# Optimization experiments

Hardware: AMD Instinct MI355X
Metric: run time of the kernel (lower is better)

Reference implementation:

```python
import jax, jax.numpy as jnp
import numpy as np

CIR_LENGTH = 64
SYM_BLK = 64
NUM_BLK = 64
H = 2 * CIR_LENGTH * SYM_BLK  # 8192, hidden size = col_num * group_size
W_SCALE = 0.01  # keep tanh out of saturation


def setup_inputs() -> dict:
    key = jax.random.key(0)
    k_x, k_ih, k_hh, k_b = jax.random.split(key, 4)
    x = jax.random.normal(k_x, (NUM_BLK, H), dtype=jnp.float32)
    W_ih = jax.random.normal(k_ih, (H, H), dtype=jnp.float32) * W_SCALE
    W_hh = jax.random.normal(k_hh, (H, H), dtype=jnp.float32) * W_SCALE
    b = jax.random.normal(k_b, (H,), dtype=jnp.float32) * W_SCALE
    return {"x": x, "W_ih": W_ih, "W_hh": W_hh, "b": b}


def reference(x, W_ih, W_hh, b):
    # Shared-weight Elman RNN over NUM_BLK blocks (the torch ModuleList holds
    # NUM copies of the SAME template module, so weights are tied).
    h0 = jnp.zeros((H,), dtype=x.dtype)

    def step(h, x_t):
        h_new = jnp.tanh(x_t @ W_ih.T + h @ W_hh.T + b)
        return h_new, h_new

    _, hs = jax.lax.scan(step, h0, x)  # hs: (NUM_BLK, H)
    # est_channel: each step's hidden reshaped to (SYM_BLK, 2*CIR_LENGTH) rows
    return hs.reshape(NUM_BLK * SYM_BLK, 2 * CIR_LENGTH)
```

## Files before the change

### kernel.cpp

```cpp
#include <hip/hip_runtime.h>
#include <cmath>
#include <type_traits>


#define HDIM 8192
#define NSTEP 64

typedef _Float16 f16;
typedef _Float16 f16x2 __attribute__((ext_vector_type(2)));
typedef _Float16 f16x4 __attribute__((ext_vector_type(4)));
typedef _Float16 f16x8 __attribute__((ext_vector_type(8)));
typedef __fp16 fp16x2_raw __attribute__((ext_vector_type(2)));
typedef float f32x4 __attribute__((ext_vector_type(4)));

#if defined(__has_builtin)
#if __has_builtin(__builtin_amdgcn_fdot2)
#define HAS_FDOT2 1
#endif
#endif

__device__ __forceinline__ f16x2 pkrtz(float a, float b) {
  fp16x2_raw r = __builtin_amdgcn_cvt_pkrtz(a, b);
  return __builtin_bit_cast(f16x2, r);
}

__device__ __forceinline__ float dot2acc(f16 a0, f16 a1, f16 b0, f16 b1, float c) {
#ifdef HAS_FDOT2
  f16x2 a = {a0, a1}, b = {b0, b1};
  return __builtin_amdgcn_fdot2(a, b, c, false);
#else
  return c + (float)a0 * (float)b0 + (float)a1 * (float)b1;
#endif
}

__global__ void cvt_f16_kernel(const float* __restrict__ src,
                               f16* __restrict__ dst, int n4) {
  int idx = blockIdx.x * blockDim.x + threadIdx.x;
  int stride = gridDim.x * blockDim.x;
  for (int i = idx; i < n4; i += stride) {
    f32x4 v = ((const f32x4*)src)[i];
    f16x4 h;
    h[0] = (f16)v[0]; h[1] = (f16)v[1]; h[2] = (f16)v[2]; h[3] = (f16)v[3];
    ((f16x4*)dst)[i] = h;
  }
}

template <bool XF16>
__global__ __launch_bounds__(256) void gemm_u_kernel(
    const float* __restrict__ x, const f16* __restrict__ x16,
    const float* __restrict__ Wih, const float* __restrict__ b,
    float* __restrict__ out) {
  const int wave = threadIdx.x >> 6;
  const int lane = threadIdx.x & 63;
  const int r = lane & 15, q = lane >> 4;
  const int n0 = blockIdx.x * 16;
  const int m0 = wave * 16;
  const float* wrow = Wih + (size_t)(n0 + r) * HDIM;
  f32x4 acc = {0.f, 0.f, 0.f, 0.f};
#pragma unroll 2
  for (int k0 = 0; k0 < HDIM; k0 += 32) {
    const int kb = k0 + q * 8;
    f16x8 fa;
    if constexpr (XF16) {
      fa = *(const f16x8*)(x16 + (size_t)(m0 + r) * HDIM + kb);
    } else {
      f32x4 a0 = *(const f32x4*)(x + (size_t)(m0 + r) * HDIM + kb);
      f32x4 a1 = *(const f32x4*)(x + (size_t)(m0 + r) * HDIM + kb + 4);
      f16x2 p0 = pkrtz(a0[0], a0[1]);
      f16x2 p1 = pkrtz(a0[2], a0[3]);
      f16x2 p2 = pkrtz(a1[0], a1[1]);
      f16x2 p3 = pkrtz(a1[2], a1[3]);
      fa = (f16x8){p0[0], p0[1], p1[0], p1[1], p2[0], p2[1], p3[0], p3[1]};
    }
    f32x4 b0 = *(const f32x4*)(wrow + kb);
    f32x4 b1 = *(const f32x4*)(wrow + kb + 4);
    f16x2 q0 = pkrtz(b0[0], b0[1]);
    f16x2 q1 = pkrtz(b0[2], b0[3]);
    f16x2 q2 = pkrtz(b1[0], b1[1]);
    f16x2 q3 = pkrtz(b1[2], b1[3]);
    f16x8 fb = {q0[0], q0[1], q1[0], q1[1], q2[0], q2[1], q3[0], q3[1]};
    acc = __builtin_amdgcn_mfma_f32_16x16x32_f16(fa, fb, acc, 0, 0, 0);
  }
  const float bv = b[n0 + r];
#pragma unroll
  for (int i = 0; i < 4; i++) {
    out[(size_t)(m0 + q * 4 + i) * HDIM + n0 + r] = acc[i] + bv;
  }
}

__global__ void step0_kernel(float* __restrict__ out) {
  int i = blockIdx.x * blockDim.x + threadIdx.x;
  out[i] = tanhf(out[i]);
}

template <bool WF16>
__global__ __launch_bounds__(1024) void step_kernel(const void* __restrict__ Wv,
                                                    float* __restrict__ out,
                                                    int t) {
  __shared__ typename std::conditional<WF16, f16, float>::type hs[HDIM];
  const float* hprev = out + (size_t)(t - 1) * HDIM;
  {
    const f32x4* hp4 = (const f32x4*)hprev;
    const int tid = threadIdx.x;
#pragma unroll
    for (int i = 0; i < HDIM / 4 / 1024; i++) {
      const int idx = i * 1024 + tid;
      f32x4 v = hp4[idx];
      if constexpr (WF16) {
        f16x4 hh;
        hh[0] = (f16)v[0]; hh[1] = (f16)v[1];
        hh[2] = (f16)v[2]; hh[3] = (f16)v[3];
        *(f16x4*)&hs[idx * 4] = hh;
      } else {
        *(f32x4*)&hs[idx * 4] = v;
      }
    }
  }
  __syncthreads();

  const int wave = threadIdx.x >> 6;
  const int lane = threadIdx.x & 63;
  const int j = blockIdx.x * 16 + wave;
  float acc = 0.f;

  if constexpr (WF16) {
    const f16* wrow = (const f16*)Wv + (size_t)j * HDIM;
#pragma unroll 4
    for (int it = 0; it < 16; it++) {
      const int kb = it * 512 + lane * 8;
      f16x8 w = *(const f16x8*)(wrow + kb);
      f16x8 h = *(const f16x8*)&hs[kb];
      acc = dot2acc(w[0], w[1], h[0], h[1], acc);
      acc = dot2acc(w[2], w[3], h[2], h[3], acc);
      acc = dot2acc(w[4], w[5], h[4], h[5], acc);
      acc = dot2acc(w[6], w[7], h[6], h[7], acc);
    }
  } else {
    const float* wrow = (const float*)Wv + (size_t)j * HDIM;
#pragma unroll 4
    for (int it = 0; it < 16; it++) {
      const int kb = it * 512 + lane * 8;
      f32x4 w0 = *(const f32x4*)(wrow + kb);
      f32x4 w1 = *(const f32x4*)(wrow + kb + 4);
      const float* hp = (const float*)&hs[kb];
      acc += w0[0] * hp[0] + w0[1] * hp[1] + w0[2] * hp[2] + w0[3] * hp[3];
      acc += w1[0] * hp[4] + w1[1] * hp[5] + w1[2] * hp[6] + w1[7 - 7 + 7] * hp[7];
    }
  }
#pragma unroll
  for (int off = 32; off >= 1; off >>= 1) acc += __shfl_down(acc, off, 64);
  if (lane == 0) {
    const float u = out[(size_t)t * HDIM + j];
    out[(size_t)t * HDIM + j] = tanhf(u + acc);
  }
}

extern "C" void kernel_launch(void* const* d_in, const int* in_sizes, int n_in,
                              void* d_out, int out_size, void* d_ws,
                              size_t ws_size, hipStream_t stream) {
  const float* x = (const float*)d_in[0];
  const float* Wih = (const float*)d_in[1];
  const float* Whh = (const float*)d_in[2];
  const float* b = (const float*)d_in[3];
  float* out = (float*)d_out;

  const size_t needW = (size_t)HDIM * HDIM * sizeof(f16);
  const size_t needX = (size_t)NSTEP * HDIM * sizeof(f16);
  const bool fast = ws_size >= needW + needX;

  if (fast) {
    f16* w16 = (f16*)d_ws;
    f16* x16 = (f16*)((char*)d_ws + needW);
    cvt_f16_kernel<<<4096, 256, 0, stream>>>(Whh, w16, HDIM * HDIM / 4);
    cvt_f16_kernel<<<64, 256, 0, stream>>>(x, x16, NSTEP * HDIM / 4);
    gemm_u_kernel<true><<<HDIM / 16, 256, 0, stream>>>(x, x16, Wih, b, out);
    step0_kernel<<<HDIM / 256, 256, 0, stream>>>(out);
    for (int t = 1; t < NSTEP; t++)
      step_kernel<true><<<HDIM / 16, 1024, 0, stream>>>((const void*)w16, out, t);
  } else {
    gemm_u_kernel<false><<<HDIM / 16, 256, 0, stream>>>(x, nullptr, Wih, b, out);
    step0_kernel<<<HDIM / 256, 256, 0, stream>>>(out);
    for (int t = 1; t < NSTEP; t++)
      step_kernel<false><<<HDIM / 16, 1024, 0, stream>>>((const void*)Whh, out, t);
  }
}
```

Before: 2.162 ms.

## Replace per-step launches with persistent kernel holding W_hh in registers and LDS

Replaces the 63 per-timestep kernel launches with one persistent kernel of 256 blocks. Each block converts its 32 rows of W_hh to fp16 once and keeps them resident, mostly in registers with the rest in LDS, so the weights are not re-read from memory every step. Steps are separated by a hierarchical atomic grid barrier, and the fp16 hidden state is double-buffered in the workspace. This removes the separate W_hh conversion pass and per-step weight traffic, but depends on all blocks being co-resident (two 512-thread blocks per CU with large LDS) and adds barrier latency on each step.

```diff
diff --git a/kernel.cpp b/kernel.cpp
--- a/kernel.cpp
+++ b/kernel.cpp
@@ -5,6 +5,14 @@
 
 #define HDIM 8192
 #define NSTEP 64
+#define GRID_P 256
+#define BLK_P 512
+#define ROWS_B 32
+#define R_W 4
+#define NCH 16
+#define NCH_REG 12
+#define NCH_LDS 4
+#define LDS_BYTES (16384 + 131072)
 
 typedef _Float16 f16;
 typedef _Float16 f16x2 __attribute__((ext_vector_type(2)));
@@ -24,13 +32,27 @@
   return __builtin_bit_cast(f16x2, r);
 }
 
-__device__ __forceinline__ float dot2acc(f16 a0, f16 a1, f16 b0, f16 b1, float c) {
+__device__ __forceinline__ float dot8(f16x8 a, f16x8 b, float c) {
 #ifdef HAS_FDOT2
-  f16x2 a = {a0, a1}, b = {b0, b1};
-  return __builtin_amdgcn_fdot2(a, b, c, false);
+  f16x2 a0 = {a[0], a[1]}, b0 = {b[0], b[1]};
+  f16x2 a1 = {a[2], a[3]}, b1 = {b[2], b[3]};
+  f16x2 a2 = {a[4], a[5]}, b2 = {b[4], b[5]};
+  f16x2 a3 = {a[6], a[7]}, b3 = {b[6], b[7]};
+  c = __builtin_amdgcn_fdot2(a0, b0, c, false);
+  c = __builtin_amdgcn_fdot2(a1, b1, c, false);
+  c = __builtin_amdgcn_fdot2(a2, b2, c, false);
+  c = __builtin_amdgcn_fdot2(a3, b3, c, false);
+  return c;
 #else
-  return c + (float)a0 * (float)b0 + (float)a1 * (float)b1;
+  for (int i = 0; i < 8; i++) c += (float)a[i] * (float)b[i];
+  return c;
 #endif
+}
+
+__device__ __forceinline__ f16x8 cvt8(f32x4 a0, f32x4 a1) {
+  f16x2 p0 = pkrtz(a0[0], a0[1]), p1 = pkrtz(a0[2], a0[3]);
+  f16x2 p2 = pkrtz(a1[0], a1[1]), p3 = pkrtz(a1[2], a1[3]);
+  return (f16x8){p0[0], p0[1], p1[0], p1[1], p2[0], p2[1], p3[0], p3[1]};
 }
 
 __global__ void cvt_f16_kernel(const float* __restrict__ src,
@@ -66,25 +88,139 @@
     } else {
       f32x4 a0 = *(const f32x4*)(x + (size_t)(m0 + r) * HDIM + kb);
       f32x4 a1 = *(const f32x4*)(x + (size_t)(m0 + r) * HDIM + kb + 4);
-      f16x2 p0 = pkrtz(a0[0], a0[1]);
-      f16x2 p1 = pkrtz(a0[2], a0[3]);
-      f16x2 p2 = pkrtz(a1[0], a1[1]);
-      f16x2 p3 = pkrtz(a1[2], a1[3]);
-      fa = (f16x8){p0[0], p0[1], p1[0], p1[1], p2[0], p2[1], p3[0], p3[1]};
+      fa = cvt8(a0, a1);
     }
     f32x4 b0 = *(const f32x4*)(wrow + kb);
     f32x4 b1 = *(const f32x4*)(wrow + kb + 4);
-    f16x2 q0 = pkrtz(b0[0], b0[1]);
-    f16x2 q1 = pkrtz(b0[2], b0[3]);
-    f16x2 q2 = pkrtz(b1[0], b1[1]);
-    f16x2 q3 = pkrtz(b1[2], b1[3]);
-    f16x8 fb = {q0[0], q0[1], q1[0], q1[1], q2[0], q2[1], q3[0], q3[1]};
+    f16x8 fb = cvt8(b0, b1);
     acc = __builtin_amdgcn_mfma_f32_16x16x32_f16(fa, fb, acc, 0, 0, 0);
   }
   const float bv = b[n0 + r];
 #pragma unroll
   for (int i = 0; i < 4; i++) {
     out[(size_t)(m0 + q * 4 + i) * HDIM + n0 + r] = acc[i] + bv;
+  }
+}
+
+__device__ __forceinline__ void gridbar(unsigned* bar, unsigned& my_gen) {
+  __syncthreads();
+  if (threadIdx.x == 0) {
+    __threadfence();
+    const unsigned target = my_gen + 1;
+    const unsigned g = blockIdx.x & 7u;
+    unsigned old = __hip_atomic_fetch_add(&bar[g * 64], 1u, __ATOMIC_ACQ_REL,
+                                          __HIP_MEMORY_SCOPE_AGENT);
+    if (old == 31u) {
+      unsigned o2 = __hip_atomic_fetch_add(&bar[576], 1u, __ATOMIC_ACQ_REL,
+                                           __HIP_MEMORY_SCOPE_AGENT);
+      if (o2 == 7u) {
+        for (int gg = 0; gg < 8; gg++)
+          __hip_atomic_store(&bar[gg * 64], 0u, __ATOMIC_RELAXED,
+                             __HIP_MEMORY_SCOPE_AGENT);
+        __hip_atomic_store(&bar[576], 0u, __ATOMIC_RELAXED,
+                           __HIP_MEMORY_SCOPE_AGENT);
+        __hip_atomic_fetch_add(&bar[640], 1u, __ATOMIC_RELEASE,
+                               __HIP_MEMORY_SCOPE_AGENT);
+      }
+    }
+    while (__hip_atomic_load(&bar[640], __ATOMIC_ACQUIRE,
+                             __HIP_MEMORY_SCOPE_AGENT) < target)
+      __builtin_amdgcn_s_sleep(2);
+  }
+  my_gen++;
+  __syncthreads();
+}
+
+extern __shared__ char smem_dyn[];
+__global__ __launch_bounds__(BLK_P, 2) void persist_kernel(
+    const float* __restrict__ Whh, float* __restrict__ out,
+    f16* __restrict__ hbuf, unsigned* __restrict__ bar) {
+  f16* h_lds = (f16*)smem_dyn;
+  f16* w_lds = (f16*)(smem_dyn + 16384);
+  const int tid = threadIdx.x;
+  const int wave = tid >> 6, lane = tid & 63;
+  const int j0 = blockIdx.x * ROWS_B;
+  const int jb = j0 + wave * R_W;
+
+  f16x8 wreg[R_W][NCH_REG];
+#pragma unroll
+  for (int r = 0; r < R_W; r++) {
+    const float* wrow = Whh + (size_t)(jb + r) * HDIM;
+#pragma unroll
+    for (int c = 0; c < NCH; c++) {
+      const int k = c * 512 + lane * 8;
+      f32x4 a0 = *(const f32x4*)(wrow + k);
+      f32x4 a1 = *(const f32x4*)(wrow + k + 4);
+      f16x8 w8 = cvt8(a0, a1);
+      if (c < NCH_REG) {
+        wreg[r][c] = w8;
+      } else {
+        const int row_l = wave * R_W + r;
+        *(f16x8*)(w_lds + ((size_t)(row_l * NCH_LDS + (c - NCH_REG)) * 64 + lane) * 8) = w8;
+      }
+    }
+  }
+
+  unsigned my_gen = 0;
+
+  if (tid < ROWS_B) {
+    const int j = j0 + tid;
+    float v = tanhf(out[j]);
+    out[j] = v;
+    hbuf[j] = (f16)v;
+  }
+  gridbar(bar, my_gen);
+
+  for (int t = 1; t < NSTEP; t++) {
+    const f16* hprev = hbuf + ((t - 1) & 1) * HDIM;
+#pragma unroll
+    for (int i = 0; i < HDIM / 8 / BLK_P; i++) {
+      const int idx = i * BLK_P + tid;
+      ((f16x8*)h_lds)[idx] = ((const f16x8*)hprev)[idx];
+    }
+    __syncthreads();
+
+    float u[R_W];
+    if (lane == 0) {
+#pragma unroll
+      for (int r = 0; r < R_W; r++) u[r] = out[(size_t)t * HDIM + jb + r];
+    }
+
+    float acc[R_W] = {0.f, 0.f, 0.f, 0.f};
+#pragma unroll
+    for (int c = 0; c < NCH_REG; c++) {
+      f16x8 hx = *(const f16x8*)(h_lds + c * 512 + lane * 8);
+#pragma unroll
+      for (int r = 0; r < R_W; r++) acc[r] = dot8(wreg[r][c], hx, acc[r]);
+    }
+#pragma unroll
+    for (int cc = 0; cc < NCH_LDS; cc++) {
+      f16x8 hx = *(const f16x8*)(h_lds + (NCH_REG + cc) * 512 + lane * 8);
+#pragma unroll
+      for (int r = 0; r < R_W; r++) {
+        const int row_l = wave * R_W + r;
+        f16x8 wl = *(const f16x8*)(w_lds + ((size_t)(row_l * NCH_LDS + cc) * 64 + lane) * 8);
+        acc[r] = dot8(wl, hx, acc[r]);
+      }
+    }
+
+#pragma unroll
+    for (int off = 32; off >= 1; off >>= 1) {
+      acc[0] += __shfl_down(acc[0], off, 64);
+      acc[1] += __shfl_down(acc[1], off, 64);
+      acc[2] += __shfl_down(acc[2], off, 64);
+      acc[3] += __shfl_down(acc[3], off, 64);
+    }
+    if (lane == 0) {
+      f16* hcur = hbuf + (t & 1) * HDIM;
+#pragma unroll
+      for (int r = 0; r < R_W; r++) {
+        float v = tanhf(u[r] + acc[r]);
+        out[(size_t)t * HDIM + jb + r] = v;
+        hcur[jb + r] = (f16)v;
+      }
+    }
+    if (t < NSTEP - 1) gridbar(bar, my_gen);
   }
 }
 
@@ -93,59 +229,31 @@
   out[i] = tanhf(out[i]);
 }
 
-template <bool WF16>
-__global__ __launch_bounds__(1024) void step_kernel(const void* __restrict__ Wv,
-                                                    float* __restrict__ out,
-                                                    int t) {
-  __shared__ typename std::conditional<WF16, f16, float>::type hs[HDIM];
+__global__ __launch_bounds__(1024) void step_kernel_f32(
+    const float* __restrict__ W, float* __restrict__ out, int t) {
+  __shared__ float hs[HDIM];
   const float* hprev = out + (size_t)(t - 1) * HDIM;
   {
     const f32x4* hp4 = (const f32x4*)hprev;
-    const int tid = threadIdx.x;
 #pragma unroll
     for (int i = 0; i < HDIM / 4 / 1024; i++) {
-      const int idx = i * 1024 + tid;
-      f32x4 v = hp4[idx];
-      if constexpr (WF16) {
-        f16x4 hh;
-        hh[0] = (f16)v[0]; hh[1] = (f16)v[1];
-        hh[2] = (f16)v[2]; hh[3] = (f16)v[3];
-        *(f16x4*)&hs[idx * 4] = hh;
-      } else {
-        *(f32x4*)&hs[idx * 4] = v;
-      }
+      const int idx = i * 1024 + threadIdx.x;
+      *(f32x4*)&hs[idx * 4] = hp4[idx];
     }
   }
   __syncthreads();
-
-  const int wave = threadIdx.x >> 6;
-  const int lane = threadIdx.x & 63;
+  const int wave = threadIdx.x >> 6, lane = threadIdx.x & 63;
   const int j = blockIdx.x * 16 + wave;
+  const float* wrow = W + (size_t)j * HDIM;
   float acc = 0.f;
-
-  if constexpr (WF16) {
-    const f16* wrow = (const f16*)Wv + (size_t)j * HDIM;
 #pragma unroll 4
-    for (int it = 0; it < 16; it++) {
-      const int kb = it * 512 + lane * 8;
-      f16x8 w = *(const f16x8*)(wrow + kb);
-      f16x8 h = *(const f16x8*)&hs[kb];
-      acc = dot2acc(w[0], w[1], h[0], h[1], acc);
-      acc = dot2acc(w[2], w[3], h[2], h[3], acc);
-      acc = dot2acc(w[4], w[5], h[4], h[5], acc);
-      acc = dot2acc(w[6], w[7], h[6], h[7], acc);
-    }
-  } else {
-    const float* wrow = (const float*)Wv + (size_t)j * HDIM;
-#pragma unroll 4
-    for (int it = 0; it < 16; it++) {
-      const int kb = it * 512 + lane * 8;
-      f32x4 w0 = *(const f32x4*)(wrow + kb);
-      f32x4 w1 = *(const f32x4*)(wrow + kb + 4);
-      const float* hp = (const float*)&hs[kb];
-      acc += w0[0] * hp[0] + w0[1] * hp[1] + w0[2] * hp[2] + w0[3] * hp[3];
-      acc += w1[0] * hp[4] + w1[1] * hp[5] + w1[2] * hp[6] + w1[7 - 7 + 7] * hp[7];
-    }
+  for (int it = 0; it < 16; it++) {
+    const int kb = it * 512 + lane * 8;
+    f32x4 w0 = *(const f32x4*)(wrow + kb);
+    f32x4 w1 = *(const f32x4*)(wrow + kb + 4);
+    const float* hp = &hs[kb];
+    acc += w0[0] * hp[0] + w0[1] * hp[1] + w0[2] * hp[2] + w0[3] * hp[3];
+    acc += w1[0] * hp[4] + w1[1] * hp[5] + w1[2] * hp[6] + w1[3] * hp[7];
   }
 #pragma unroll
   for (int off = 32; off >= 1; off >>= 1) acc += __shfl_down(acc, off, 64);
@@ -164,23 +272,21 @@
   const float* b = (const float*)d_in[3];
   float* out = (float*)d_out;
 
-  const size_t needW = (size_t)HDIM * HDIM * sizeof(f16);
-  const size_t needX = (size_t)NSTEP * HDIM * sizeof(f16);
-  const bool fast = ws_size >= needW + needX;
-
-  if (fast) {
-    f16* w16 = (f16*)d_ws;
-    f16* x16 = (f16*)((char*)d_ws + needW);
-    cvt_f16_kernel<<<4096, 256, 0, stream>>>(Whh, w16, HDIM * HDIM / 4);
+  const size_t need = 65536 + (size_t)NSTEP * HDIM * sizeof(f16);
+  if (ws_size >= need) {
+    unsigned* bar = (unsigned*)d_ws;
+    f16* hbuf = (f16*)((char*)d_ws + 4096);
+    f16* x16 = (f16*)((char*)d_ws + 65536);
+    hipMemsetAsync(d_ws, 0, 4096, stream);
     cvt_f16_kernel<<<64, 256, 0, stream>>>(x, x16, NSTEP * HDIM / 4);
     gemm_u_kernel<true><<<HDIM / 16, 256, 0, stream>>>(x, x16, Wih, b, out);
-    step0_kernel<<<HDIM / 256, 256, 0, stream>>>(out);
-    for (int t = 1; t < NSTEP; t++)
-      step_kernel<true><<<HDIM / 16, 1024, 0, stream>>>((const void*)w16, out, t);
+    hipFuncSetAttribute((const void*)persist_kernel,
+                        hipFuncAttributeMaxDynamicSharedMemorySize, LDS_BYTES);
+    persist_kernel<<<GRID_P, BLK_P, LDS_BYTES, stream>>>(Whh, out, hbuf, bar);
   } else {
     gemm_u_kernel<false><<<HDIM / 16, 256, 0, stream>>>(x, nullptr, Wih, b, out);
     step0_kernel<<<HDIM / 256, 256, 0, stream>>>(out);
     for (int t = 1; t < NSTEP; t++)
-      step_kernel<false><<<HDIM / 16, 1024, 0, stream>>>((const void*)Whh, out, t);
-  }
-}
+      step_kernel_f32<<<HDIM / 16, 1024, 0, stream>>>(Whh, out, t);
+  }
+}
```

New measurement: 2.218 ms. 1.03x slower.
